# Performance work log

Measured on AMD Instinct MI355X. Metric: run time of the kernel, lower is better.

Reference implementation:

```python
import jax, jax.numpy as jnp
import numpy as np

N_TOKEN = 1024
N_I = 512
VOCAB = 10
D = 1024
L = 12
H_MLP = 4096
EPS = 1e-5  # torch LayerNorm default
B = 8


def layer_norm(x, g, b):
    mu = jnp.mean(x, axis=-1, keepdims=True)
    var = jnp.mean(jnp.square(x - mu), axis=-1, keepdims=True)
    return (x - mu) * jax.lax.rsqrt(var + EPS) * g + b


def setup_inputs() -> dict:
    key = jax.random.key(0)
    ks = jax.random.split(key, 12)
    s = 0.02  # init scale for weights
    return {
        'xt': jax.random.randint(ks[0], (B, N_TOKEN - N_I), 0, VOCAB),
        'zi': jax.random.randint(ks[1], (B, N_I), 0, VOCAB),
        'pos_emb': jax.random.normal(ks[2], (N_TOKEN, D), jnp.float32) * s,
        't_emb': jax.random.normal(ks[3], (VOCAB, D), jnp.float32) * s,
        'Wq': jax.random.normal(ks[4], (L, D, D), jnp.float32) * s,
        'Wk': jax.random.normal(ks[5], (L, D, D), jnp.float32) * s,
        'Wv': jax.random.normal(ks[6], (L, D, D), jnp.float32) * s,
        'ln1_g': jnp.ones((L, D), jnp.float32),
        'ln1_b': jnp.zeros((L, D), jnp.float32),
        'ln2_g': jnp.ones((L, D), jnp.float32),
        'ln2_b': jnp.zeros((L, D), jnp.float32),
        'mlp_w1': jax.random.normal(ks[7], (L, D, H_MLP), jnp.float32) * s,
        'mlp_b1': jnp.zeros((L, H_MLP), jnp.float32),
        'mlp_w2': jax.random.normal(ks[8], (L, H_MLP, D), jnp.float32) * s,
        'mlp_b2': jnp.zeros((L, D), jnp.float32),
        'ro_w': jax.random.normal(ks[9], (D, 1), jnp.float32) * s,
        'ro_b': jnp.zeros((1,), jnp.float32),
    }


def _forward(xt, zi, pos_emb, t_emb, Wq, Wk, Wv, ln1_g, ln1_b, ln2_g, ln2_b,
             mlp_w1, mlp_b1, mlp_w2, mlp_b2, ro_w, ro_b):
    # token embeddings: image tokens get -(c - zi)^2/2 in the first VOCAB dims, 0 elsewhere
    opts = jnp.arange(VOCAB, dtype=jnp.float32)
    leave = -jnp.square(opts[None, None, :] - zi[:, :, None].astype(jnp.float32)) * 0.5  # [B, N_I, V]
    emb_i = jnp.pad(leave, ((0, 0), (0, 0), (0, D - VOCAB)))  # [B, N_I, D]
    emb_t = t_emb[xt]                                          # [B, T1, D]
    H = jnp.concatenate([emb_i, emb_t], axis=1) + pos_emb[None, :, :]  # [B, T, D]

    inv_sqrt_d = np.float32(1.0 / np.sqrt(D))

    def step(H, p):
        wq, wk, wv, g1, b1, g2, b2, w1, bb1, w2, bb2 = p
        H1 = layer_norm(H, g1, b1)
        q = H1 @ wq
        k = H1 @ wk
        v = H1 @ wv
        attn = jnp.einsum('bid,bjd->bij', q, k) * inv_sqrt_d  # [B, T, T]
        attn = jax.nn.softmax(attn, axis=-1)
        H = H + jnp.einsum('bij,bjd->bid', attn, v)
        H2 = layer_norm(H, g2, b2)
        # torch nn.GELU default is exact (erf) gelu
        H = H + (jax.nn.gelu(H2 @ w1 + bb1, approximate=False) @ w2 + bb2)
        return H, None

    H, _ = jax.lax.scan(step, H, (Wq, Wk, Wv, ln1_g, ln1_b, ln2_g, ln2_b,
                                  mlp_w1, mlp_b1, mlp_w2, mlp_b2))
    pred = H @ ro_w + ro_b  # [B, T, 1]
    return pred[:, :N_I, 0]  # [B, N_I]


def reference(xt, zi, pos_emb, t_emb, Wq, Wk, Wv, ln1_g, ln1_b, ln2_g, ln2_b,
              mlp_w1, mlp_b1, mlp_w2, mlp_b2, ro_w, ro_b):
    return _forward(xt, zi, pos_emb, t_emb, Wq, Wk, Wv, ln1_g, ln1_b, ln2_g, ln2_b,
                    mlp_w1, mlp_b1, mlp_w2, mlp_b2, ro_w, ro_b)
```

## Files before the change

kernel.cpp:

```cpp
#include <hip/hip_runtime.h>
#include <cstdint>
#include <cmath>

typedef unsigned short u16;
typedef unsigned int u32;
typedef short bf16x8 __attribute__((ext_vector_type(8)));
typedef float f32x4 __attribute__((ext_vector_type(4)));

#define DEV static __device__ __forceinline__

DEV u16 f2bf(float f) {
  union { float f; u32 u; } v; v.f = f;
  return (u16)((v.u + 0x7FFFu + ((v.u >> 16) & 1u)) >> 16);
}
DEV float bf2f(u32 lo16) {
  union { u32 u; float f; } v; v.u = lo16 << 16; return v.f;
}

DEV void gload16(const void* g, u16* l) {
  __builtin_amdgcn_global_load_lds(
      (const __attribute__((address_space(1))) void*)g,
      (__attribute__((address_space(3))) void*)l, 16, 0, 0);
}

template<int MODE>
__global__ __launch_bounds__(256)
void gemmA(const u16* __restrict__ A, const u16* __restrict__ Bt,
           void* __restrict__ Cv, const float* __restrict__ bias,
           int M, int N, int K, int ldA, int ldB,
           long sA, long sB, long sC, float scale)
{
  __shared__ __align__(16) u16 As[128 * 64];
  __shared__ __align__(16) u16 Bs[128 * 64];

  const int bz = blockIdx.z;
  const long m0 = (long)blockIdx.x * 128, n0 = (long)blockIdx.y * 128;
  const int t = threadIdx.x;
  const int wave = t >> 6, lane = t & 63;
  const int wr = (wave >> 1) * 64, wc = (wave & 1) * 64;
  const int lg = lane >> 4, lr = lane & 15;

  const long ldA2 = (long)ldA * 2, ldB2 = (long)ldB * 2;

  const int rl = lane >> 3, c7 = lane & 7;
  const int sb = (c7 * 16) ^ (rl << 4);
  const char* aP[4]; const char* bP[4];
  u16* aL[4]; u16* bL[4];
  {
    const char* Ab = (const char*)(A + (long)bz * sA);
    const char* Bb = (const char*)(Bt + (long)bz * sB);
    #pragma unroll
    for (int c = 0; c < 4; ++c) {
      const int q = c * 4 + wave;
      aP[c] = Ab + (m0 + q * 8 + rl) * ldA2 + sb;
      bP[c] = Bb + (n0 + q * 8 + rl) * ldB2 + sb;
      aL[c] = As + q * 512;
      bL[c] = Bs + q * 512;
    }
  }

  const int rswz = (lr & 7) << 4;
  auto rd = [&](const u16* base, int row, int cbyte) -> bf16x8 {
    return *reinterpret_cast<const bf16x8*>(
        reinterpret_cast<const char*>(base) + row * 128 + (cbyte ^ rswz));
  };

  f32x4 acc[4][4];
  #pragma unroll
  for (int i = 0; i < 4; ++i)
    #pragma unroll
    for (int j = 0; j < 4; ++j)
      acc[i][j] = (f32x4){0.f, 0.f, 0.f, 0.f};

  for (int k0 = 0; k0 < K; k0 += 64) {
    #pragma unroll
    for (int c = 0; c < 4; ++c) {
      gload16(aP[c], aL[c]);
      gload16(bP[c], bL[c]);
      aP[c] += 128; bP[c] += 128;
    }
    __syncthreads();

    #pragma unroll
    for (int ks = 0; ks < 2; ++ks) {
      bf16x8 a[4], b[4];
      #pragma unroll
      for (int i = 0; i < 4; ++i)
        a[i] = rd(As, wr + i * 16 + lr, ks * 64 + lg * 16);
      #pragma unroll
      for (int i = 0; i < 4; ++i)
        b[i] = rd(Bs, wc + i * 16 + lr, ks * 64 + lg * 16);
      #pragma unroll
      for (int mi = 0; mi < 4; ++mi)
        #pragma unroll
        for (int ni = 0; ni < 4; ++ni)
          acc[mi][ni] = __builtin_amdgcn_mfma_f32_16x16x32_bf16(a[mi], b[ni], acc[mi][ni], 0, 0, 0);
    }
    __syncthreads();
  }

  #pragma unroll
  for (int mi = 0; mi < 4; ++mi) {
    #pragma unroll
    for (int ni = 0; ni < 4; ++ni) {
      #pragma unroll
      for (int r = 0; r < 4; ++r) {
        const long grow = m0 + wr + mi * 16 + lg * 4 + r;
        const long gcol = n0 + wc + ni * 16 + lr;
        const float v = acc[mi][ni][r];
        if constexpr (MODE == 0) {
          u16* Cp = (u16*)Cv + (long)bz * sC;
          Cp[grow * N + gcol] = f2bf(v * scale);
        } else if constexpr (MODE == 2) {
          float* Cp = (float*)Cv + (long)bz * sC;
          Cp[grow * N + gcol] += v;
        } else if constexpr (MODE == 3) {
          u16* Cp = (u16*)Cv + (long)bz * sC;
          const float x = v + bias[gcol];
          const float ge = 0.5f * x * (1.0f + erff(x * 0.70710678118f));
          Cp[grow * N + gcol] = f2bf(ge);
        } else if constexpr (MODE == 4) {
          float* Cp = (float*)Cv + (long)bz * sC;
          const long idx = grow * N + gcol;
          Cp[idx] = Cp[idx] + v + bias[gcol];
        }
      }
    }
  }
}

__global__ __launch_bounds__(256)
void trans_k(const float* __restrict__ wq, const float* __restrict__ wk,
             const float* __restrict__ wv, const float* __restrict__ w1,
             const float* __restrict__ w2, u16* __restrict__ ob)
{
  __shared__ u16 T[64][68];
  const int b = blockIdx.x;
  const float* in; u16* out; int K, N, tk, tn;
  if (b < 768) {
    const int m = b >> 8, tt = b & 255;
    in = (m == 0) ? wq : (m == 1) ? wk : wv;
    out = ob + (long)m * 1048576L;
    K = 1024; N = 1024; tk = tt >> 4; tn = tt & 15;
  } else if (b < 1792) {
    const int tt = b - 768;
    in = w1; out = ob + 3L * 1048576L; K = 1024; N = 4096;
    tk = tt >> 6; tn = tt & 63;
  } else {
    const int tt = b - 1792;
    in = w2; out = ob + 7L * 1048576L; K = 4096; N = 1024;
    tk = tt >> 4; tn = tt & 15;
  }
  const int k0 = tk * 64, n0 = tn * 64;
  const int t = threadIdx.x;
  {
    const int r = t >> 2, cq = (t & 3) * 16;
    const float* src = in + (long)(k0 + r) * N + n0 + cq;
    #pragma unroll
    for (int q = 0; q < 4; ++q) {
      const float4 v = *reinterpret_cast<const float4*>(src + q * 4);
      T[r][cq + q * 4 + 0] = f2bf(v.x);
      T[r][cq + q * 4 + 1] = f2bf(v.y);
      T[r][cq + q * 4 + 2] = f2bf(v.z);
      T[r][cq + q * 4 + 3] = f2bf(v.w);
    }
  }
  __syncthreads();
  {
    const int n = t >> 2, kq2 = (t & 3) * 16;
    u16 tmp[16];
    #pragma unroll
    for (int j = 0; j < 16; ++j) tmp[j] = T[kq2 + j][n];
    uint4* dst = reinterpret_cast<uint4*>(out + (long)(n0 + n) * K + k0 + kq2);
    dst[0] = *reinterpret_cast<const uint4*>(&tmp[0]);
    dst[1] = *reinterpret_cast<const uint4*>(&tmp[8]);
  }
}

__global__ __launch_bounds__(256)
void embed_k(const int* __restrict__ xt, const int* __restrict__ zi,
             const float* __restrict__ pos, const float* __restrict__ temb,
             float* __restrict__ H)
{
  const int bt = blockIdx.x;
  const int b = bt >> 10, tk = bt & 1023;
  const int d = threadIdx.x * 4;
  const float4 p = reinterpret_cast<const float4*>(pos + (long)tk * 1024)[threadIdx.x];
  float4 v;
  if (tk < 512) {
    const float z = (float)zi[b * 512 + tk];
    const float c0 = (float)(d + 0) - z, c1 = (float)(d + 1) - z;
    const float c2 = (float)(d + 2) - z, c3 = (float)(d + 3) - z;
    v.x = (d + 0 < 10) ? -0.5f * c0 * c0 : 0.f;
    v.y = (d + 1 < 10) ? -0.5f * c1 * c1 : 0.f;
    v.z = (d + 2 < 10) ? -0.5f * c2 * c2 : 0.f;
    v.w = (d + 3 < 10) ? -0.5f * c3 * c3 : 0.f;
  } else {
    const float* te = temb + (long)xt[b * 512 + (tk - 512)] * 1024;
    v = reinterpret_cast<const float4*>(te)[threadIdx.x];
  }
  float4 o; o.x = v.x + p.x; o.y = v.y + p.y; o.z = v.z + p.z; o.w = v.w + p.w;
  reinterpret_cast<float4*>(H + (long)bt * 1024)[threadIdx.x] = o;
}

__global__ __launch_bounds__(256)
void ln_k(const float* __restrict__ X, const float* __restrict__ g,
          const float* __restrict__ bta, u16* __restrict__ Y)
{
  __shared__ float sm[8];
  const long row = blockIdx.x;
  const float4 x = reinterpret_cast<const float4*>(X + row * 1024)[threadIdx.x];
  float s1 = x.x + x.y + x.z + x.w;
  float s2 = x.x * x.x + x.y * x.y + x.z * x.z + x.w * x.w;
  #pragma unroll
  for (int o = 32; o > 0; o >>= 1) { s1 += __shfl_down(s1, o); s2 += __shfl_down(s2, o); }
  const int w = threadIdx.x >> 6, ln = threadIdx.x & 63;
  if (ln == 0) { sm[w] = s1; sm[4 + w] = s2; }
  __syncthreads();
  s1 = sm[0] + sm[1] + sm[2] + sm[3];
  s2 = sm[4] + sm[5] + sm[6] + sm[7];
  const float mu = s1 * (1.f / 1024.f);
  const float var = s2 * (1.f / 1024.f) - mu * mu;
  const float inv = rsqrtf(var + 1e-5f);
  const float4 gg = reinterpret_cast<const float4*>(g)[threadIdx.x];
  const float4 bb = reinterpret_cast<const float4*>(bta)[threadIdx.x];
  const u32 o0 = (u32)f2bf((x.x - mu) * inv * gg.x + bb.x) | ((u32)f2bf((x.y - mu) * inv * gg.y + bb.y) << 16);
  const u32 o1 = (u32)f2bf((x.z - mu) * inv * gg.z + bb.z) | ((u32)f2bf((x.w - mu) * inv * gg.w + bb.w) << 16);
  reinterpret_cast<uint2*>(Y + row * 1024)[threadIdx.x] = make_uint2(o0, o1);
}

__global__ __launch_bounds__(256)
void sm_k(const u16* __restrict__ S, u16* __restrict__ P)
{
  __shared__ float sm[8];
  const long row = blockIdx.x;
  const uint2 raw = reinterpret_cast<const uint2*>(S + row * 1024)[threadIdx.x];
  const float x0 = bf2f(raw.x & 0xffffu), x1 = bf2f(raw.x >> 16);
  const float x2 = bf2f(raw.y & 0xffffu), x3 = bf2f(raw.y >> 16);
  float m = fmaxf(fmaxf(x0, x1), fmaxf(x2, x3));
  #pragma unroll
  for (int o = 32; o > 0; o >>= 1) m = fmaxf(m, __shfl_down(m, o));
  const int w = threadIdx.x >> 6, ln = threadIdx.x & 63;
  if (ln == 0) sm[w] = m;
  __syncthreads();
  m = fmaxf(fmaxf(sm[0], sm[1]), fmaxf(sm[2], sm[3]));
  const float e0 = __expf(x0 - m), e1 = __expf(x1 - m);
  const float e2 = __expf(x2 - m), e3 = __expf(x3 - m);
  float s = e0 + e1 + e2 + e3;
  #pragma unroll
  for (int o = 32; o > 0; o >>= 1) s += __shfl_down(s, o);
  if (ln == 0) sm[4 + w] = s;
  __syncthreads();
  const float tot = sm[4] + sm[5] + sm[6] + sm[7];
  const float r = 1.0f / tot;
  const u32 o0 = (u32)f2bf(e0 * r) | ((u32)f2bf(e1 * r) << 16);
  const u32 o1 = (u32)f2bf(e2 * r) | ((u32)f2bf(e3 * r) << 16);
  reinterpret_cast<uint2*>(P + row * 1024)[threadIdx.x] = make_uint2(o0, o1);
}

__global__ __launch_bounds__(256)
void ro_k(const float* __restrict__ H, const float* __restrict__ w,
          const float* __restrict__ b, float* __restrict__ out)
{
  __shared__ float sm[4];
  const int row = blockIdx.x;
  const int bb = row >> 9, i = row & 511;
  const float* h = H + ((long)bb * 1024 + i) * 1024;
  const float4 x = reinterpret_cast<const float4*>(h)[threadIdx.x];
  const float4 ww = reinterpret_cast<const float4*>(w)[threadIdx.x];
  float s = x.x * ww.x + x.y * ww.y + x.z * ww.z + x.w * ww.w;
  #pragma unroll
  for (int o = 32; o > 0; o >>= 1) s += __shfl_down(s, o);
  const int wv = threadIdx.x >> 6, ln = threadIdx.x & 63;
  if (ln == 0) sm[wv] = s;
  __syncthreads();
  if (threadIdx.x == 0) out[row] = sm[0] + sm[1] + sm[2] + sm[3] + b[0];
}

extern "C" void kernel_launch(void* const* d_in, const int* in_sizes, int n_in,
                              void* d_out, int out_size, void* d_ws, size_t ws_size,
                              hipStream_t stream)
{
  const int* xt = (const int*)d_in[0];
  const int* zi = (const int*)d_in[1];
  const float* pos  = (const float*)d_in[2];
  const float* temb = (const float*)d_in[3];
  const float* Wq = (const float*)d_in[4];
  const float* Wk = (const float*)d_in[5];
  const float* Wv = (const float*)d_in[6];
  const float* ln1g = (const float*)d_in[7];
  const float* ln1b = (const float*)d_in[8];
  const float* ln2g = (const float*)d_in[9];
  const float* ln2b = (const float*)d_in[10];
  const float* w1 = (const float*)d_in[11];
  const float* b1 = (const float*)d_in[12];
  const float* w2 = (const float*)d_in[13];
  const float* b2 = (const float*)d_in[14];
  const float* row_w = (const float*)d_in[15];
  const float* row_b = (const float*)d_in[16];

  char* ws = (char*)d_ws;
  const long MB = 1024 * 1024;
  float* H   = (float*)(ws + 0);
  u16*   H1  = (u16*)(ws + 32 * MB);
  u16*   QK  = (u16*)(ws + 48 * MB);
  u16*   Vt  = (u16*)(ws + 80 * MB);
  u16*   S   = (u16*)(ws + 96 * MB);
  u16*   P   = (u16*)(ws + 112 * MB);
  u16*   G   = (u16*)(ws + 80 * MB);
  u16*   WT  = (u16*)(ws + 144 * MB);

  u16* WvT = WT + 2 * 1048576L;
  u16* W1T = WT + 3 * 1048576L;
  u16* W2T = WT + 7 * 1048576L;

  const long s1M = 1024L * 1024L;
  const long s2M = 2L * 1024L * 1024L;

  embed_k<<<8192, 256, 0, stream>>>(xt, zi, pos, temb, H);

  for (int l = 0; l < 12; ++l) {
    const float* wq = Wq + (long)l * s1M;
    const float* wk = Wk + (long)l * s1M;
    const float* wv = Wv + (long)l * s1M;
    const float* mw1 = w1 + (long)l * 1024L * 4096L;
    const float* mb1 = b1 + (long)l * 4096L;
    const float* mw2 = w2 + (long)l * 4096L * 1024L;
    const float* mb2 = b2 + (long)l * 1024L;

    trans_k<<<2816, 256, 0, stream>>>(wq, wk, wv, mw1, mw2, WT);

    ln_k<<<8192, 256, 0, stream>>>(H, ln1g + l * 1024, ln1b + l * 1024, H1);

    gemmA<0><<<dim3(64, 16, 1), 256, 0, stream>>>(H1, WT, QK, nullptr,
        8192, 2048, 1024, 1024, 1024, 0, 0, 0, 1.f);
    gemmA<0><<<dim3(8, 8, 8), 256, 0, stream>>>(WvT, H1, Vt, nullptr,
        1024, 1024, 1024, 1024, 1024, 0, s1M, s1M, 1.f);

    gemmA<0><<<dim3(8, 8, 8), 256, 0, stream>>>(QK, QK + 1024, S, nullptr,
        1024, 1024, 1024, 2048, 2048, s2M, s2M, s1M, 1.f / 32.f);

    sm_k<<<8192, 256, 0, stream>>>(S, P);

    gemmA<2><<<dim3(8, 8, 8), 256, 0, stream>>>(P, Vt, (void*)H, nullptr,
        1024, 1024, 1024, 1024, 1024, s1M, s1M, s1M, 1.f);

    ln_k<<<8192, 256, 0, stream>>>(H, ln2g + l * 1024, ln2b + l * 1024, H1);

    gemmA<3><<<dim3(64, 32, 1), 256, 0, stream>>>(H1, W1T, G, mb1,
        8192, 4096, 1024, 1024, 1024, 0, 0, 0, 1.f);
    gemmA<4><<<dim3(64, 8, 1), 256, 0, stream>>>(G, W2T, (void*)H, mb2,
        8192, 1024, 4096, 4096, 4096, 0, 0, 0, 1.f);
  }

  ro_k<<<4096, 256, 0, stream>>>(H, row_w, row_b, (float*)d_out);
}
```

Baseline: 4.290 ms.

## Add 256x256-tile 512-thread GEMM for QK and MLP-up projections

Adds a new GEMM kernel, gemmW, that uses 256x256 output tiles with 8 waves. Each wave computes a 128x64 sub-tile with 32 MFMA accumulators, and LDS reads use XOR-swizzled addressing. The kernel replaces the smaller-tile gemmA for the fused Q/K projection and the MLP first layer with GELU epilogue, aiming to raise arithmetic intensity and cut global/LDS traffic per FLOP. It keeps a single-buffered loop with two barriers per K step, uses heavy register pressure (128 accumulator floats per thread), and launches fewer blocks, all of which may limit occupancy and latency hiding.

```diff
diff --git a/kernel.cpp b/kernel.cpp
--- a/kernel.cpp
+++ b/kernel.cpp
@@ -129,6 +129,101 @@
   }
 }
 
+template<int MODE>
+__global__ __launch_bounds__(512)
+void gemmW(const u16* __restrict__ A, const u16* __restrict__ Bt,
+           void* __restrict__ Cv, const float* __restrict__ bias,
+           int M, int N, int K, int ldA, int ldB, float scale)
+{
+  __shared__ __align__(16) u16 As[256 * 64];
+  __shared__ __align__(16) u16 Bs[256 * 64];
+
+  const long m0 = (long)blockIdx.x * 256, n0 = (long)blockIdx.y * 256;
+  const int t = threadIdx.x;
+  const int wave = t >> 6, lane = t & 63;
+  const int wrg = wave >> 2, wcg = wave & 3;
+  const int lg = lane >> 4, lr = lane & 15;
+
+  const long ldA2 = (long)ldA * 2, ldB2 = (long)ldB * 2;
+
+  const int rl = lane >> 3, c7 = lane & 7;
+  const int sb = (c7 * 16) ^ (rl << 4);
+  const char* aP[4]; const char* bP[4];
+  u16* aL[4]; u16* bL[4];
+  {
+    const char* Ab = (const char*)A;
+    const char* Bb = (const char*)Bt;
+    #pragma unroll
+    for (int c = 0; c < 4; ++c) {
+      const int q = c * 8 + wave;
+      aP[c] = Ab + (m0 + q * 8 + rl) * ldA2 + sb;
+      bP[c] = Bb + (n0 + q * 8 + rl) * ldB2 + sb;
+      aL[c] = As + q * 512;
+      bL[c] = Bs + q * 512;
+    }
+  }
+
+  const int rswz = (lr & 7) << 4;
+  auto rd = [&](const u16* base, int row, int cbyte) -> bf16x8 {
+    return *reinterpret_cast<const bf16x8*>(
+        reinterpret_cast<const char*>(base) + row * 128 + (cbyte ^ rswz));
+  };
+
+  f32x4 acc[8][4];
+  #pragma unroll
+  for (int i = 0; i < 8; ++i)
+    #pragma unroll
+    for (int j = 0; j < 4; ++j)
+      acc[i][j] = (f32x4){0.f, 0.f, 0.f, 0.f};
+
+  for (int k0 = 0; k0 < K; k0 += 64) {
+    #pragma unroll
+    for (int c = 0; c < 4; ++c) {
+      gload16(aP[c], aL[c]);
+      gload16(bP[c], bL[c]);
+      aP[c] += 128; bP[c] += 128;
+    }
+    __syncthreads();
+
+    #pragma unroll
+    for (int ks = 0; ks < 2; ++ks) {
+      bf16x8 a[8], b[4];
+      #pragma unroll
+      for (int i = 0; i < 8; ++i)
+        a[i] = rd(As, wrg * 128 + i * 16 + lr, ks * 64 + lg * 16);
+      #pragma unroll
+      for (int i = 0; i < 4; ++i)
+        b[i] = rd(Bs, wcg * 64 + i * 16 + lr, ks * 64 + lg * 16);
+      #pragma unroll
+      for (int mi = 0; mi < 8; ++mi)
+        #pragma unroll
+        for (int ni = 0; ni < 4; ++ni)
+          acc[mi][ni] = __builtin_amdgcn_mfma_f32_16x16x32_bf16(a[mi], b[ni], acc[mi][ni], 0, 0, 0);
+    }
+    __syncthreads();
+  }
+
+  #pragma unroll
+  for (int mi = 0; mi < 8; ++mi) {
+    #pragma unroll
+    for (int ni = 0; ni < 4; ++ni) {
+      #pragma unroll
+      for (int r = 0; r < 4; ++r) {
+        const long grow = m0 + wrg * 128 + mi * 16 + lg * 4 + r;
+        const long gcol = n0 + wcg * 64 + ni * 16 + lr;
+        const float v = acc[mi][ni][r];
+        if constexpr (MODE == 0) {
+          ((u16*)Cv)[grow * N + gcol] = f2bf(v * scale);
+        } else if constexpr (MODE == 3) {
+          const float x = v + bias[gcol];
+          const float ge = 0.5f * x * (1.0f + erff(x * 0.70710678118f));
+          ((u16*)Cv)[grow * N + gcol] = f2bf(ge);
+        }
+      }
+    }
+  }
+}
+
 __global__ __launch_bounds__(256)
 void trans_k(const float* __restrict__ wq, const float* __restrict__ wk,
              const float* __restrict__ wv, const float* __restrict__ w1,
@@ -332,8 +427,8 @@
 
     ln_k<<<8192, 256, 0, stream>>>(H, ln1g + l * 1024, ln1b + l * 1024, H1);
 
-    gemmA<0><<<dim3(64, 16, 1), 256, 0, stream>>>(H1, WT, QK, nullptr,
-        8192, 2048, 1024, 1024, 1024, 0, 0, 0, 1.f);
+    gemmW<0><<<dim3(32, 8, 1), 512, 0, stream>>>(H1, WT, QK, nullptr,
+        8192, 2048, 1024, 1024, 1024, 1.f);
     gemmA<0><<<dim3(8, 8, 8), 256, 0, stream>>>(WvT, H1, Vt, nullptr,
         1024, 1024, 1024, 1024, 1024, 0, s1M, s1M, 1.f);
 
@@ -347,8 +442,8 @@
 
     ln_k<<<8192, 256, 0, stream>>>(H, ln2g + l * 1024, ln2b + l * 1024, H1);
 
-    gemmA<3><<<dim3(64, 32, 1), 256, 0, stream>>>(H1, W1T, G, mb1,
-        8192, 4096, 1024, 1024, 1024, 0, 0, 0, 1.f);
+    gemmW<3><<<dim3(32, 16, 1), 512, 0, stream>>>(H1, W1T, G, mb1,
+        8192, 4096, 1024, 1024, 1024, 1.f);
     gemmA<4><<<dim3(64, 8, 1), 256, 0, stream>>>(G, W2T, (void*)H, mb2,
         8192, 1024, 4096, 4096, 4096, 0, 0, 0, 1.f);
   }
```

After: 4.980 ms. 16.1% more time.
